# Optimization experiments

Hardware: AMD Instinct MI355X
Metric: run time of the kernel (lower is better)

## Reference

```python
import jax, jax.numpy as jnp
import numpy as np

B, S, D, E, TOP_K = 4, 4096, 2048, 64, 2

def setup_inputs() -> dict:
    key = jax.random.key(0)
    k1, k2, k3, k4 = jax.random.split(key, 4)
    return {
        "mh_output": jax.random.normal(k1, (B, S, D), dtype=jnp.float32),
        "W_route": jax.random.normal(k2, (D, E), dtype=jnp.float32) * (1.0 / np.sqrt(D)),
        "b_route": jnp.zeros((E,), dtype=jnp.float32),
        "W_noise": jax.random.normal(k3, (D, E), dtype=jnp.float32) * (1.0 / np.sqrt(D)),
        "b_noise": jnp.zeros((E,), dtype=jnp.float32),
        "noise": jax.random.normal(k4, (B, S, E), dtype=jnp.float32),
    }

def reference(mh_output, W_route, b_route, W_noise, b_noise, noise):
    # logits / noise logits: [B, S, E]
    logits = jnp.einsum("bsd,de->bse", mh_output, W_route) + b_route
    noise_logits = jnp.einsum("bsd,de->bse", mh_output, W_noise) + b_noise
    noisy_logits = logits + noise * jax.nn.softplus(noise_logits)

    top_vals, indices = jax.lax.top_k(noisy_logits, TOP_K)  # [B,S,K]

    # scatter top-k values into a -inf-filled tensor, then softmax
    flat_vals = top_vals.reshape(-1, TOP_K)
    flat_idx = indices.reshape(-1, TOP_K)
    n_tok = flat_idx.shape[0]
    rows = jnp.arange(n_tok)[:, None]
    sparse = jnp.full((n_tok, E), -jnp.inf, dtype=noisy_logits.dtype)
    sparse = sparse.at[rows, flat_idx].set(flat_vals)
    probs = jax.nn.softmax(sparse, axis=-1).reshape(noisy_logits.shape)
    return probs, indices
```

## Files before the change

### kernel.cpp

```cpp
#include <hip/hip_runtime.h>
#include <math.h>

#define M_TOK 16384
#define D_DIM 2048
#define E_EXP 64
#define NCOL  128
#define BM    64
#define BK    64
#define NITER (D_DIM / BK)

#define ROW_STRIDE 144
#define PLANE (BM * ROW_STRIDE)
#define BUFSZ (3 * PLANE)
#define SMEM_BYTES (2 * BUFSZ)

typedef float  f32x4  __attribute__((ext_vector_type(4)));
typedef short  bf16x8 __attribute__((ext_vector_type(8)));

#define MFMA_B16(a, b, c) __builtin_amdgcn_mfma_f32_16x16x32_bf16((a), (b), (c), 0, 0, 0)

__device__ __forceinline__ unsigned short bfrne(float f) {
    unsigned int u = __float_as_uint(f);
    return (unsigned short)((u + 0x7fffu + ((u >> 16) & 1u)) >> 16);
}
__device__ __forceinline__ float bfhi(unsigned short h) {
    return __uint_as_float((unsigned int)h << 16);
}

__device__ __forceinline__ bool beats(float va, int ia, float vb, int ib) {
    return (va > vb) || (va == vb && ia < ib);
}

__global__ __launch_bounds__(256) void prep_w(
    const float* __restrict__ Wr, const float* __restrict__ Wn,
    unsigned short* __restrict__ Wg)
{
    const int g    = blockIdx.x * 256 + threadIdx.x;
    const int lane = g & 63;
    const int cf   = (g >> 6) & 7;
    const int kblk = g >> 9;
    const int colL = (cf & 3) * 16 + (lane & 15);
    const float* __restrict__ W = (cf < 4) ? Wr : Wn;
    const int kbase = kblk * 32 + (lane >> 4) * 8;

    bf16x8 o0, o1, o2;
    #pragma unroll
    for (int j = 0; j < 8; ++j) {
        const float w = W[(size_t)(kbase + j) * E_EXP + colL];
        const unsigned short h0 = bfrne(w);
        const float r  = w - bfhi(h0);
        const unsigned short h1 = bfrne(r);
        const float r2 = r - bfhi(h1);
        const unsigned short h2 = bfrne(r2);
        o0[j] = (short)h0; o1[j] = (short)h1; o2[j] = (short)h2;
    }
    const size_t s0 = (((size_t)kblk * 3 + 0) * 8 + cf) * 64 + lane;
    const size_t s1 = (((size_t)kblk * 3 + 1) * 8 + cf) * 64 + lane;
    const size_t s2 = (((size_t)kblk * 3 + 2) * 8 + cf) * 64 + lane;
    *(bf16x8*)(Wg + s0 * 8) = o0;
    *(bf16x8*)(Wg + s1 * 8) = o1;
    *(bf16x8*)(Wg + s2 * 8) = o2;
}

__device__ __forceinline__ void load_b(const unsigned short* __restrict__ Wg,
                                       int it, int wc, int lane,
                                       bf16x8 (&Bv)[2][2][3])
{
    #pragma unroll
    for (int s = 0; s < 2; ++s) {
        const int kblk = it * 2 + s;
        #pragma unroll
        for (int cfi = 0; cfi < 2; ++cfi) {
            #pragma unroll
            for (int p = 0; p < 3; ++p) {
                const size_t idx = (((size_t)kblk * 3 + p) * 8 + (wc * 2 + cfi)) * 64 + lane;
                Bv[s][cfi][p] = *(const bf16x8*)(Wg + idx * 8);
            }
        }
    }
}

__device__ __forceinline__ void load_a(const float* __restrict__ A, int tokBase,
                                       int it, int tid, float4& x, float4& y)
{
    const int row = tid >> 3;
    const int kc8 = tid & 7;
    const float* g = A + (size_t)(tokBase + row) * D_DIM + it * BK + kc8 * 8;
    x = *(const float4*)(g);
    y = *(const float4*)(g + 4);
}

__device__ __forceinline__ void split8(const float4& a, const float4& b,
                                       bf16x8& o0, bf16x8& o1, bf16x8& o2)
{
    const float v[8] = {a.x, a.y, a.z, a.w, b.x, b.y, b.z, b.w};
    #pragma unroll
    for (int j = 0; j < 8; ++j) {
        const unsigned short h0 = bfrne(v[j]);
        const float r  = v[j] - bfhi(h0);
        const unsigned short h1 = bfrne(r);
        const float r2 = r - bfhi(h1);
        const unsigned short h2 = bfrne(r2);
        o0[j] = (short)h0; o1[j] = (short)h1; o2[j] = (short)h2;
    }
}

__device__ __forceinline__ void cvt_store(char* smem, int buf, int tid,
                                          const float4& x, const float4& y)
{
    bf16x8 h0, h1, h2;
    split8(x, y, h0, h1, h2);
    const int row = tid >> 3;
    const int kc8 = tid & 7;
    char* base = smem + buf * BUFSZ + row * ROW_STRIDE + kc8 * 16;
    *(bf16x8*)(base)             = h0;
    *(bf16x8*)(base + PLANE)     = h1;
    *(bf16x8*)(base + 2 * PLANE) = h2;
}

__device__ __forceinline__ void compute_iter(const char* Ab, int wr, int lane,
                                             const bf16x8 (&Bc)[2][2][3],
                                             f32x4 (&acch)[2][2], f32x4 (&accl)[2][2])
{
    #pragma unroll
    for (int s = 0; s < 2; ++s) {
        bf16x8 a0[2], a1[2], a2[2];
        #pragma unroll
        for (int rf = 0; rf < 2; ++rf) {
            const int row = wr * 32 + rf * 16 + (lane & 15);
            const int off = row * ROW_STRIDE + (s * 4 + (lane >> 4)) * 16;
            a0[rf] = *(const bf16x8*)(Ab + off);
            a1[rf] = *(const bf16x8*)(Ab + PLANE + off);
            a2[rf] = *(const bf16x8*)(Ab + 2 * PLANE + off);
        }
        #pragma unroll
        for (int cfi = 0; cfi < 2; ++cfi) {
            #pragma unroll
            for (int rf = 0; rf < 2; ++rf) {
                acch[rf][cfi] = MFMA_B16(a0[rf], Bc[s][cfi][0], acch[rf][cfi]);
                accl[rf][cfi] = MFMA_B16(a0[rf], Bc[s][cfi][1], accl[rf][cfi]);
                accl[rf][cfi] = MFMA_B16(a1[rf], Bc[s][cfi][0], accl[rf][cfi]);
                accl[rf][cfi] = MFMA_B16(a1[rf], Bc[s][cfi][1], accl[rf][cfi]);
                accl[rf][cfi] = MFMA_B16(a0[rf], Bc[s][cfi][2], accl[rf][cfi]);
                accl[rf][cfi] = MFMA_B16(a2[rf], Bc[s][cfi][0], accl[rf][cfi]);
            }
        }
    }
}

__global__ __launch_bounds__(512, 1) void fused_router(
    const float* __restrict__ A,
    const unsigned short* __restrict__ Wg,
    const float* __restrict__ br, const float* __restrict__ bn,
    const float* __restrict__ noise,
    float* __restrict__ probs, float* __restrict__ idxo)
{
    __shared__ __align__(16) char smem[SMEM_BYTES];

    const int tid  = threadIdx.x;
    const int lane = tid & 63;
    const int wid  = tid >> 6;
    const int wr   = wid >> 2;
    const int wc   = wid & 3;
    const int tokBase = blockIdx.x * BM;

    f32x4 acch[2][2], accl[2][2];
    const f32x4 zero4 = {0.f, 0.f, 0.f, 0.f};
    #pragma unroll
    for (int a = 0; a < 2; ++a)
        #pragma unroll
        for (int b = 0; b < 2; ++b) { acch[a][b] = zero4; accl[a][b] = zero4; }

    bf16x8 B0[2][2][3], B1[2][2][3];
    float4 xE, yE, xO, yO;

    load_a(A, tokBase, 0, tid, xE, yE);
    load_b(Wg, 0, wc, lane, B0);
    load_a(A, tokBase, 1, tid, xO, yO);
    cvt_store(smem, 0, tid, xE, yE);
    __syncthreads();

    #pragma unroll 1
    for (int it2 = 0; it2 < NITER / 2; ++it2) {
        const int ita = it2 * 2;
        const int itb = ita + 1;

        load_b(Wg, itb, wc, lane, B1);
        cvt_store(smem, 1, tid, xO, yO);
        if (ita + 2 < NITER) load_a(A, tokBase, ita + 2, tid, xE, yE);
        compute_iter(smem, wr, lane, B0, acch, accl);
        __syncthreads();

        if (itb + 1 < NITER) load_b(Wg, itb + 1, wc, lane, B0);
        if (ita + 2 < NITER) cvt_store(smem, 0, tid, xE, yE);
        if (itb + 2 < NITER) load_a(A, tokBase, itb + 2, tid, xO, yO);
        compute_iter(smem + BUFSZ, wr, lane, B1, acch, accl);
        __syncthreads();
    }

    float (*Llds)[NCOL + 1] = (float (*)[NCOL + 1])smem;
    #pragma unroll
    for (int rf = 0; rf < 2; ++rf) {
        #pragma unroll
        for (int cfi = 0; cfi < 2; ++cfi) {
            const int col  = wc * 32 + cfi * 16 + (lane & 15);
            const int rowb = wr * 32 + rf * 16 + (lane >> 4) * 4;
            #pragma unroll
            for (int r = 0; r < 4; ++r)
                Llds[rowb + r][col] = acch[rf][cfi][r] + accl[rf][cfi][r];
        }
    }
    __syncthreads();

    const int token = tid >> 3;
    const int s8    = tid & 7;
    const int tokG  = tokBase + token;

    float v0 = -INFINITY, v1 = -INFINITY;
    int i0 = 0, i1 = 0;
    const float* nz = noise + (size_t)tokG * E_EXP + s8 * 8;
    #pragma unroll
    for (int j = 0; j < 8; ++j) {
        const int e = s8 * 8 + j;
        const float lg = Llds[token][e]      + br[e];
        const float nl = Llds[token][64 + e] + bn[e];
        const float sp = fmaxf(nl, 0.0f) + log1pf(expf(-fabsf(nl)));
        const float v  = fmaf(nz[j], sp, lg);
        if (beats(v, e, v0, i0))      { v1 = v0; i1 = i0; v0 = v; i0 = e; }
        else if (beats(v, e, v1, i1)) { v1 = v;  i1 = e; }
    }
    #pragma unroll
    for (int m = 1; m < 8; m <<= 1) {
        const float w0 = __shfl_xor(v0, m), w1 = __shfl_xor(v1, m);
        const int   j0 = __shfl_xor(i0, m), j1 = __shfl_xor(i1, m);
        if (beats(v0, i0, w0, j0)) {
            if (!beats(v1, i1, w0, j0)) { v1 = w0; i1 = j0; }
        } else {
            if (beats(v0, i0, w1, j1)) { v1 = v0; i1 = i0; }
            else                       { v1 = w1; i1 = j1; }
            v0 = w0; i0 = j0;
        }
    }
    const float e1  = expf(v1 - v0);
    const float den = 1.0f + e1;
    const float p0 = 1.0f / den;
    const float p1 = e1 / den;

    float out[8];
    #pragma unroll
    for (int j = 0; j < 8; ++j) {
        const int e = s8 * 8 + j;
        out[j] = (e == i0) ? p0 : ((e == i1) ? p1 : 0.0f);
    }
    float* pb = probs + (size_t)tokG * E_EXP + s8 * 8;
    *(float4*)(pb)     = make_float4(out[0], out[1], out[2], out[3]);
    *(float4*)(pb + 4) = make_float4(out[4], out[5], out[6], out[7]);
    if (s8 == 0)
        *(float2*)(idxo + (size_t)tokG * 2) = make_float2((float)i0, (float)i1);
}

extern "C" void kernel_launch(void* const* d_in, const int* in_sizes, int n_in,
                              void* d_out, int out_size, void* d_ws, size_t ws_size,
                              hipStream_t stream) {
    (void)in_sizes; (void)n_in; (void)out_size; (void)ws_size;
    const float* A  = (const float*)d_in[0];
    const float* Wr = (const float*)d_in[1];
    const float* br = (const float*)d_in[2];
    const float* Wn = (const float*)d_in[3];
    const float* bn = (const float*)d_in[4];
    const float* nz = (const float*)d_in[5];

    float* probs = (float*)d_out;
    float* idxo  = probs + (size_t)M_TOK * E_EXP;

    unsigned short* Wg = (unsigned short*)d_ws;

    prep_w<<<128, 256, 0, stream>>>(Wr, Wn, Wg);
    fused_router<<<M_TOK / BM, 512, 0, stream>>>(A, Wg, br, bn, nz, probs, idxo);
}
```

Measured before the change: 235.6 us.

## Halve token tile to 32 rows, raise occupancy, cheapen bf16 split conversion

Shrinks the per-block token tile from 64 to 32 rows, so each wave owns one 16-row fragment. The grid doubles and launch bounds allow up to 4 blocks per SM, aiming to hide load and MFMA latency better with more resident waves. The first two bf16 split terms now use truncation instead of round-to-nearest, which makes conversion cheaper while the third RNE term keeps the residual accurate. The epilogue is remapped to 16 threads per token with vectorised float4 loads. In exchange, the weight fragments are reloaded for every 32 tokens instead of every 64, which doubles L2 traffic for W.

```diff
diff --git a/kernel.cpp b/kernel.cpp
--- a/kernel.cpp
+++ b/kernel.cpp
@@ -5,7 +5,7 @@
 #define D_DIM 2048
 #define E_EXP 64
 #define NCOL  128
-#define BM    64
+#define BM    32
 #define BK    64
 #define NITER (D_DIM / BK)
 
@@ -14,8 +14,9 @@
 #define BUFSZ (3 * PLANE)
 #define SMEM_BYTES (2 * BUFSZ)
 
-typedef float  f32x4  __attribute__((ext_vector_type(4)));
-typedef short  bf16x8 __attribute__((ext_vector_type(8)));
+typedef float         f32x4  __attribute__((ext_vector_type(4)));
+typedef short         bf16x8 __attribute__((ext_vector_type(8)));
+typedef unsigned int  uint;
 
 #define MFMA_B16(a, b, c) __builtin_amdgcn_mfma_f32_16x16x32_bf16((a), (b), (c), 0, 0, 0)
 
@@ -81,74 +82,67 @@
 }
 
 __device__ __forceinline__ void load_a(const float* __restrict__ A, int tokBase,
-                                       int it, int tid, float4& x, float4& y)
-{
-    const int row = tid >> 3;
-    const int kc8 = tid & 7;
-    const float* g = A + (size_t)(tokBase + row) * D_DIM + it * BK + kc8 * 8;
-    x = *(const float4*)(g);
-    y = *(const float4*)(g + 4);
-}
-
-__device__ __forceinline__ void split8(const float4& a, const float4& b,
-                                       bf16x8& o0, bf16x8& o1, bf16x8& o2)
-{
-    const float v[8] = {a.x, a.y, a.z, a.w, b.x, b.y, b.z, b.w};
-    #pragma unroll
-    for (int j = 0; j < 8; ++j) {
-        const unsigned short h0 = bfrne(v[j]);
-        const float r  = v[j] - bfhi(h0);
-        const unsigned short h1 = bfrne(r);
-        const float r2 = r - bfhi(h1);
-        const unsigned short h2 = bfrne(r2);
-        o0[j] = (short)h0; o1[j] = (short)h1; o2[j] = (short)h2;
-    }
-}
-
-__device__ __forceinline__ void cvt_store(char* smem, int buf, int tid,
-                                          const float4& x, const float4& y)
-{
-    bf16x8 h0, h1, h2;
-    split8(x, y, h0, h1, h2);
-    const int row = tid >> 3;
-    const int kc8 = tid & 7;
-    char* base = smem + buf * BUFSZ + row * ROW_STRIDE + kc8 * 16;
-    *(bf16x8*)(base)             = h0;
-    *(bf16x8*)(base + PLANE)     = h1;
-    *(bf16x8*)(base + 2 * PLANE) = h2;
+                                       int it, int tid, float4& x)
+{
+    const int row = tid >> 4;
+    const int kc  = tid & 15;
+    x = *(const float4*)(A + (size_t)(tokBase + row) * D_DIM + it * BK + kc * 4);
+}
+
+__device__ __forceinline__ void cvt_store(char* smem, int buf, int tid, const float4& x)
+{
+    const float v[4] = {x.x, x.y, x.z, x.w};
+    uint t0[4], t1[4]; unsigned short h2[4];
+    #pragma unroll
+    for (int j = 0; j < 4; ++j) {
+        const uint u = __float_as_uint(v[j]);
+        t0[j] = u & 0xffff0000u;
+        const float r = v[j] - __uint_as_float(t0[j]);
+        const uint ru = __float_as_uint(r);
+        t1[j] = ru & 0xffff0000u;
+        const float r2 = r - __uint_as_float(t1[j]);
+        h2[j] = bfrne(r2);
+    }
+    uint2 w0, w1, w2;
+    w0.x = (t0[0] >> 16) | t0[1];  w0.y = (t0[2] >> 16) | t0[3];
+    w1.x = (t1[0] >> 16) | t1[1];  w1.y = (t1[2] >> 16) | t1[3];
+    w2.x = (uint)h2[0] | ((uint)h2[1] << 16);
+    w2.y = (uint)h2[2] | ((uint)h2[3] << 16);
+
+    const int row = tid >> 4;
+    const int kc  = tid & 15;
+    char* base = smem + buf * BUFSZ + row * ROW_STRIDE + kc * 8;
+    *(uint2*)(base)             = w0;
+    *(uint2*)(base + PLANE)     = w1;
+    *(uint2*)(base + 2 * PLANE) = w2;
 }
 
 __device__ __forceinline__ void compute_iter(const char* Ab, int wr, int lane,
                                              const bf16x8 (&Bc)[2][2][3],
-                                             f32x4 (&acch)[2][2], f32x4 (&accl)[2][2])
+                                             f32x4 (&acch)[2], f32x4 (&accl)[2])
 {
     #pragma unroll
     for (int s = 0; s < 2; ++s) {
-        bf16x8 a0[2], a1[2], a2[2];
-        #pragma unroll
-        for (int rf = 0; rf < 2; ++rf) {
-            const int row = wr * 32 + rf * 16 + (lane & 15);
-            const int off = row * ROW_STRIDE + (s * 4 + (lane >> 4)) * 16;
-            a0[rf] = *(const bf16x8*)(Ab + off);
-            a1[rf] = *(const bf16x8*)(Ab + PLANE + off);
-            a2[rf] = *(const bf16x8*)(Ab + 2 * PLANE + off);
-        }
+        const int row = wr * 16 + (lane & 15);
+        const int off = row * ROW_STRIDE + (s * 4 + (lane >> 4)) * 16;
+        const bf16x8 a0 = *(const bf16x8*)(Ab + off);
+        const bf16x8 a1 = *(const bf16x8*)(Ab + PLANE + off);
+        const bf16x8 a2 = *(const bf16x8*)(Ab + 2 * PLANE + off);
         #pragma unroll
         for (int cfi = 0; cfi < 2; ++cfi) {
-            #pragma unroll
-            for (int rf = 0; rf < 2; ++rf) {
-                acch[rf][cfi] = MFMA_B16(a0[rf], Bc[s][cfi][0], acch[rf][cfi]);
-                accl[rf][cfi] = MFMA_B16(a0[rf], Bc[s][cfi][1], accl[rf][cfi]);
-                accl[rf][cfi] = MFMA_B16(a1[rf], Bc[s][cfi][0], accl[rf][cfi]);
-                accl[rf][cfi] = MFMA_B16(a1[rf], Bc[s][cfi][1], accl[rf][cfi]);
-                accl[rf][cfi] = MFMA_B16(a0[rf], Bc[s][cfi][2], accl[rf][cfi]);
-                accl[rf][cfi] = MFMA_B16(a2[rf], Bc[s][cfi][0], accl[rf][cfi]);
-            }
-        }
-    }
-}
-
-__global__ __launch_bounds__(512, 1) void fused_router(
+            acch[cfi] = MFMA_B16(a0, Bc[s][cfi][0], acch[cfi]);
+            accl[cfi] = MFMA_B16(a0, Bc[s][cfi][1], accl[cfi]);
+            accl[cfi] = MFMA_B16(a1, Bc[s][cfi][0], accl[cfi]);
+            accl[cfi] = MFMA_B16(a1, Bc[s][cfi][1], accl[cfi]);
+            accl[cfi] = MFMA_B16(a0, Bc[s][cfi][2], accl[cfi]);
+            accl[cfi] = MFMA_B16(a2, Bc[s][cfi][0], accl[cfi]);
+        }
+    }
+}
+
+#define LL_LD 132
+
+__global__ __launch_bounds__(512, 4) void fused_router(
     const float* __restrict__ A,
     const unsigned short* __restrict__ Wg,
     const float* __restrict__ br, const float* __restrict__ bn,
@@ -164,20 +158,17 @@
     const int wc   = wid & 3;
     const int tokBase = blockIdx.x * BM;
 
-    f32x4 acch[2][2], accl[2][2];
+    f32x4 acch[2], accl[2];
     const f32x4 zero4 = {0.f, 0.f, 0.f, 0.f};
-    #pragma unroll
-    for (int a = 0; a < 2; ++a)
-        #pragma unroll
-        for (int b = 0; b < 2; ++b) { acch[a][b] = zero4; accl[a][b] = zero4; }
+    acch[0] = zero4; acch[1] = zero4; accl[0] = zero4; accl[1] = zero4;
 
     bf16x8 B0[2][2][3], B1[2][2][3];
-    float4 xE, yE, xO, yO;
-
-    load_a(A, tokBase, 0, tid, xE, yE);
+    float4 xE, xO;
+
+    load_a(A, tokBase, 0, tid, xE);
     load_b(Wg, 0, wc, lane, B0);
-    load_a(A, tokBase, 1, tid, xO, yO);
-    cvt_store(smem, 0, tid, xE, yE);
+    load_a(A, tokBase, 1, tid, xO);
+    cvt_store(smem, 0, tid, xE);
     __syncthreads();
 
     #pragma unroll 1
@@ -186,51 +177,59 @@
         const int itb = ita + 1;
 
         load_b(Wg, itb, wc, lane, B1);
-        cvt_store(smem, 1, tid, xO, yO);
-        if (ita + 2 < NITER) load_a(A, tokBase, ita + 2, tid, xE, yE);
+        cvt_store(smem, 1, tid, xO);
+        if (ita + 2 < NITER) load_a(A, tokBase, ita + 2, tid, xE);
         compute_iter(smem, wr, lane, B0, acch, accl);
         __syncthreads();
 
         if (itb + 1 < NITER) load_b(Wg, itb + 1, wc, lane, B0);
-        if (ita + 2 < NITER) cvt_store(smem, 0, tid, xE, yE);
-        if (itb + 2 < NITER) load_a(A, tokBase, itb + 2, tid, xO, yO);
+        if (ita + 2 < NITER) cvt_store(smem, 0, tid, xE);
+        if (itb + 2 < NITER) load_a(A, tokBase, itb + 2, tid, xO);
         compute_iter(smem + BUFSZ, wr, lane, B1, acch, accl);
         __syncthreads();
     }
 
-    float (*Llds)[NCOL + 1] = (float (*)[NCOL + 1])smem;
-    #pragma unroll
-    for (int rf = 0; rf < 2; ++rf) {
-        #pragma unroll
-        for (int cfi = 0; cfi < 2; ++cfi) {
-            const int col  = wc * 32 + cfi * 16 + (lane & 15);
-            const int rowb = wr * 32 + rf * 16 + (lane >> 4) * 4;
-            #pragma unroll
-            for (int r = 0; r < 4; ++r)
-                Llds[rowb + r][col] = acch[rf][cfi][r] + accl[rf][cfi][r];
-        }
+    float (*Llds)[LL_LD] = (float (*)[LL_LD])smem;
+    #pragma unroll
+    for (int cfi = 0; cfi < 2; ++cfi) {
+        const int col  = wc * 32 + cfi * 16 + (lane & 15);
+        const int rowb = wr * 16 + (lane >> 4) * 4;
+        #pragma unroll
+        for (int r = 0; r < 4; ++r)
+            Llds[rowb + r][col] = acch[cfi][r] + accl[cfi][r];
     }
     __syncthreads();
 
-    const int token = tid >> 3;
-    const int s8    = tid & 7;
+    const int token = tid >> 4;
+    const int s16   = tid & 15;
     const int tokG  = tokBase + token;
 
     float v0 = -INFINITY, v1 = -INFINITY;
     int i0 = 0, i1 = 0;
-    const float* nz = noise + (size_t)tokG * E_EXP + s8 * 8;
-    #pragma unroll
-    for (int j = 0; j < 8; ++j) {
-        const int e = s8 * 8 + j;
-        const float lg = Llds[token][e]      + br[e];
-        const float nl = Llds[token][64 + e] + bn[e];
-        const float sp = fmaxf(nl, 0.0f) + log1pf(expf(-fabsf(nl)));
-        const float v  = fmaf(nz[j], sp, lg);
-        if (beats(v, e, v0, i0))      { v1 = v0; i1 = i0; v0 = v; i0 = e; }
-        else if (beats(v, e, v1, i1)) { v1 = v;  i1 = e; }
-    }
-    #pragma unroll
-    for (int m = 1; m < 8; m <<= 1) {
+    {
+        const float4 n4 = *(const float4*)(noise + (size_t)tokG * E_EXP + s16 * 4);
+        const float4 b4 = *(const float4*)(br + s16 * 4);
+        const float4 c4 = *(const float4*)(bn + s16 * 4);
+        const float4 l4 = *(const float4*)(&Llds[token][s16 * 4]);
+        const float4 m4 = *(const float4*)(&Llds[token][64 + s16 * 4]);
+        const float nv[4] = {n4.x, n4.y, n4.z, n4.w};
+        const float bv[4] = {b4.x, b4.y, b4.z, b4.w};
+        const float cv[4] = {c4.x, c4.y, c4.z, c4.w};
+        const float lv[4] = {l4.x, l4.y, l4.z, l4.w};
+        const float mv[4] = {m4.x, m4.y, m4.z, m4.w};
+        #pragma unroll
+        for (int j = 0; j < 4; ++j) {
+            const int e = s16 * 4 + j;
+            const float lg = lv[j] + bv[j];
+            const float nl = mv[j] + cv[j];
+            const float sp = fmaxf(nl, 0.0f) + log1pf(expf(-fabsf(nl)));
+            const float v  = fmaf(nv[j], sp, lg);
+            if (beats(v, e, v0, i0))      { v1 = v0; i1 = i0; v0 = v; i0 = e; }
+            else if (beats(v, e, v1, i1)) { v1 = v;  i1 = e; }
+        }
+    }
+    #pragma unroll
+    for (int m = 1; m < 16; m <<= 1) {
         const float w0 = __shfl_xor(v0, m), w1 = __shfl_xor(v1, m);
         const int   j0 = __shfl_xor(i0, m), j1 = __shfl_xor(i1, m);
         if (beats(v0, i0, w0, j0)) {
@@ -246,16 +245,15 @@
     const float p0 = 1.0f / den;
     const float p1 = e1 / den;
 
-    float out[8];
-    #pragma unroll
-    for (int j = 0; j < 8; ++j) {
-        const int e = s8 * 8 + j;
+    float out[4];
+    #pragma unroll
+    for (int j = 0; j < 4; ++j) {
+        const int e = s16 * 4 + j;
         out[j] = (e == i0) ? p0 : ((e == i1) ? p1 : 0.0f);
     }
-    float* pb = probs + (size_t)tokG * E_EXP + s8 * 8;
-    *(float4*)(pb)     = make_float4(out[0], out[1], out[2], out[3]);
-    *(float4*)(pb + 4) = make_float4(out[4], out[5], out[6], out[7]);
-    if (s8 == 0)
+    *(float4*)(probs + (size_t)tokG * E_EXP + s16 * 4) =
+        make_float4(out[0], out[1], out[2], out[3]);
+    if (s16 == 0)
         *(float2*)(idxo + (size_t)tokG * 2) = make_float2((float)i0, (float)i1);
 }
 
```

Result: slower. 426.0 us (+80.8%).
